# Optimization experiments

Measured on AMD Instinct MI355X. Metric: run time of the kernel, lower is better.

Reference implementation:

```python
import jax, jax.numpy as jnp
import numpy as np

B, S, H = 2, 1024, 4096
N, NOPE, ROPE, V = 64, 128, 64, 128
KV_LORA, Q_LORA = 512, 1536
QK = NOPE + ROPE  # 192
MAXPOS = 4096
SCALE = QK ** -0.5
EPS = 1e-6


def rmsnorm(x, w, eps=EPS):
    var = jnp.mean(jnp.square(x.astype(jnp.float32)), axis=-1, keepdims=True)
    return (x.astype(jnp.float32) * jax.lax.rsqrt(var + eps)).astype(x.dtype) * w


def rotate_half(x):
    x1, x2 = jnp.split(x, 2, axis=-1)
    return jnp.concatenate([-x2, x1], axis=-1)


def setup_inputs() -> dict:
    key = jax.random.key(0)
    ks = jax.random.split(key, 8)
    hidden_states = jax.random.normal(ks[0], (B, S, H), dtype=jnp.float32)
    position_ids = jnp.tile(jnp.arange(S, dtype=jnp.int64)[None, :], (B, 1))
    # real RoPE tables
    inv_freq = 1.0 / (10000.0 ** (np.arange(0, ROPE, 2, dtype=np.float32) / ROPE))
    t = np.arange(MAXPOS, dtype=np.float32)
    freqs = np.outer(t, inv_freq)
    emb = np.concatenate([freqs, freqs], axis=-1)
    cos = jnp.asarray(np.cos(emb), dtype=jnp.float32)
    sin = jnp.asarray(np.sin(emb), dtype=jnp.float32)
    def lin(k, out_f, in_f):
        return jax.random.normal(k, (out_f, in_f), dtype=jnp.float32) * (in_f ** -0.5)
    return {
        'hidden_states': hidden_states,
        'position_ids': position_ids,
        'cos': cos,
        'sin': sin,
        'q_a_w': lin(ks[1], Q_LORA, H),
        'q_a_ln_w': jnp.ones((Q_LORA,), dtype=jnp.float32),
        'q_b_w': lin(ks[2], N * QK, Q_LORA),
        'kv_a_w': lin(ks[3], KV_LORA + ROPE, H),
        'kv_a_ln_w': jnp.ones((KV_LORA,), dtype=jnp.float32),
        'kv_b_w': lin(ks[4], N * (NOPE + V), KV_LORA),
        'o_w': lin(ks[5], H, N * V),
    }


def reference(hidden_states, position_ids, cos, sin, q_a_w, q_a_ln_w, q_b_w,
              kv_a_w, kv_a_ln_w, kv_b_w, o_w):
    b, s, _ = hidden_states.shape
    # Q path: low-rank down-proj -> RMSNorm -> up-proj
    q = rmsnorm(hidden_states @ q_a_w.T, q_a_ln_w) @ q_b_w.T
    q = q.reshape(b, s, N, QK)
    q_nope, q_pe = q[..., :NOPE], q[..., NOPE:]          # [b,s,n,128],[b,s,n,64]
    # KV path: joint down-proj -> split latent / rope part
    kv_a = hidden_states @ kv_a_w.T                       # [b,s,512+64]
    compressed_kv = rmsnorm(kv_a[..., :KV_LORA], kv_a_ln_w)  # [b,s,512]
    k_pe = kv_a[..., KV_LORA:].reshape(b, s, 1, ROPE)
    # RoPE with explicit cos/sin gathered by position_ids (unsqueeze head dim=2)
    cos_p = cos[position_ids][:, :, None, :]              # [b,s,1,64]
    sin_p = sin[position_ids][:, :, None, :]
    q_pe = q_pe * cos_p + rotate_half(q_pe) * sin_p
    k_pe = k_pe * cos_p + rotate_half(k_pe) * sin_p
    k_pe = k_pe[:, :, 0, :]                               # [b,s,64]
    # Absorbed kv_b weights: W_UK [n,128,512], W_UV [n,128,512]
    W = kv_b_w.reshape(N, NOPE + V, KV_LORA)
    W_UK, W_UV = W[:, :NOPE], W[:, NOPE:]
    # Absorb W_UK into q: attention operates in latent space
    q_lat = jnp.einsum('bsnd,ndc->bsnc', q_nope, W_UK)    # [b,s,n,512]
    scores = jnp.einsum('bsnc,btc->bnst', q_lat, compressed_kv)
    scores = scores + jnp.einsum('bsnd,btd->bnst', q_pe, k_pe)
    scores = scores * SCALE
    causal = jnp.tril(jnp.ones((s, s), dtype=bool))
    scores = jnp.where(causal[None, None], scores, jnp.finfo(scores.dtype).min)
    attn = jax.nn.softmax(scores, axis=-1)                # [b,n,s,t]
    out_lat = jnp.einsum('bnst,btc->bsnc', attn, compressed_kv)
    out = jnp.einsum('bsnc,nvc->bsnv', out_lat, W_UV)     # [b,s,n,128]
    out = out.reshape(b, s, N * V) @ o_w.T
    return out
```

## Files before the change

### kernel.cpp

```cpp
#include <hip/hip_runtime.h>
#include <hip/hip_bf16.h>
#include <math.h>


#define SCALE_QK 0.07216878364870322f

typedef short bf16x8 __attribute__((ext_vector_type(8)));
typedef float f32x4  __attribute__((ext_vector_type(4)));

__global__ __launch_bounds__(256) void cast_f32_bf16(
    const float* __restrict__ src, __hip_bfloat16* __restrict__ dst, long n)
{
    long i = ((long)blockIdx.x * 256 + threadIdx.x) * 8;
    if (i >= n) return;
    float4 a = *(const float4*)(src + i);
    float4 b = *(const float4*)(src + i + 4);
    union { bf16x8 v; __hip_bfloat16 h[8]; } u;
    u.h[0] = __float2bfloat16(a.x); u.h[1] = __float2bfloat16(a.y);
    u.h[2] = __float2bfloat16(a.z); u.h[3] = __float2bfloat16(a.w);
    u.h[4] = __float2bfloat16(b.x); u.h[5] = __float2bfloat16(b.y);
    u.h[6] = __float2bfloat16(b.z); u.h[7] = __float2bfloat16(b.w);
    *(bf16x8*)(dst + i) = u.v;
}

__global__ __launch_bounds__(256) void cast_pad_kvaw(
    const float* __restrict__ src, __hip_bfloat16* __restrict__ dst)
{
    long i = ((long)blockIdx.x * 256 + threadIdx.x) * 8;
    if (i >= 640L * 4096) return;
    const int row = (int)(i >> 12);
    union { bf16x8 v; __hip_bfloat16 h[8]; } u;
    if (row < 576) {
        float4 a = *(const float4*)(src + i);
        float4 b = *(const float4*)(src + i + 4);
        u.h[0] = __float2bfloat16(a.x); u.h[1] = __float2bfloat16(a.y);
        u.h[2] = __float2bfloat16(a.z); u.h[3] = __float2bfloat16(a.w);
        u.h[4] = __float2bfloat16(b.x); u.h[5] = __float2bfloat16(b.y);
        u.h[6] = __float2bfloat16(b.z); u.h[7] = __float2bfloat16(b.w);
    } else {
        for (int j = 0; j < 8; ++j) u.h[j] = __float2bfloat16(0.f);
    }
    *(bf16x8*)(dst + i) = u.v;
}

template<int OUT_BF16>
__global__ __launch_bounds__(256) void gemm_bf16(
    const __hip_bfloat16* __restrict__ A, const __hip_bfloat16* __restrict__ B,
    void* __restrict__ Cv, int M, int N, int K)
{
    __shared__ __hip_bfloat16 Asm[128 * 32];
    __shared__ __hip_bfloat16 Bsm[128 * 32];
    const int t  = threadIdx.x;
    const int w  = t >> 6, l = t & 63;
    const int wr = w >> 1, wc = w & 1;
    const int lr = l & 15, g = l >> 4;
    const int m0 = blockIdx.y * 128, n0 = blockIdx.x * 128;
    const int srow = l >> 2;
    const int schk = l & 3;

    f32x4 acc[4][4] = {};

    for (int k0 = 0; k0 < K; k0 += 32) {
#pragma unroll
        for (int i = 0; i < 2; ++i) {
            const int ia = w * 2 + i;
            const __hip_bfloat16* ga = A + (size_t)(m0 + ia * 16 + srow) * K + k0 + schk * 8;
            __builtin_amdgcn_global_load_lds(
                (const __attribute__((address_space(1))) void*)ga,
                (__attribute__((address_space(3))) void*)(Asm + ia * 512), 16, 0, 0);
            const __hip_bfloat16* gb = B + (size_t)(n0 + ia * 16 + srow) * K + k0 + schk * 8;
            __builtin_amdgcn_global_load_lds(
                (const __attribute__((address_space(1))) void*)gb,
                (__attribute__((address_space(3))) void*)(Bsm + ia * 512), 16, 0, 0);
        }
        __syncthreads();
        bf16x8 af[4], bfr[4];
#pragma unroll
        for (int fi = 0; fi < 4; ++fi)
            af[fi] = *(const bf16x8*)(Asm + (wr * 64 + fi * 16 + lr) * 32 + g * 8);
#pragma unroll
        for (int fj = 0; fj < 4; ++fj)
            bfr[fj] = *(const bf16x8*)(Bsm + (wc * 64 + fj * 16 + lr) * 32 + g * 8);
#pragma unroll
        for (int fi = 0; fi < 4; ++fi)
#pragma unroll
            for (int fj = 0; fj < 4; ++fj)
                acc[fi][fj] = __builtin_amdgcn_mfma_f32_16x16x32_bf16(
                    af[fi], bfr[fj], acc[fi][fj], 0, 0, 0);
        __syncthreads();
    }

#pragma unroll
    for (int fi = 0; fi < 4; ++fi)
#pragma unroll
        for (int fj = 0; fj < 4; ++fj) {
            const int col = n0 + wc * 64 + fj * 16 + lr;
#pragma unroll
            for (int r = 0; r < 4; ++r) {
                const size_t row = (size_t)(m0 + wr * 64 + fi * 16 + g * 4 + r);
                if (OUT_BF16)
                    ((__hip_bfloat16*)Cv)[row * N + col] = __float2bfloat16(acc[fi][fj][r]);
                else
                    ((float*)Cv)[row * N + col] = acc[fi][fj][r];
            }
        }
}

__global__ __launch_bounds__(256) void rmsnorm_qa(
    const float* __restrict__ x, const float* __restrict__ w,
    __hip_bfloat16* __restrict__ o)
{
    __shared__ float red[4];
    const int row = blockIdx.x;
    const float* xr = x + (size_t)row * 1536;
    float ss = 0.f;
#pragma unroll
    for (int i = threadIdx.x; i < 1536; i += 256) { float v = xr[i]; ss = fmaf(v, v, ss); }
#pragma unroll
    for (int off = 1; off < 64; off <<= 1) ss += __shfl_xor(ss, off, 64);
    const int lane = threadIdx.x & 63, wid = threadIdx.x >> 6;
    if (lane == 0) red[wid] = ss;
    __syncthreads();
    ss = red[0] + red[1] + red[2] + red[3];
    const float r = rsqrtf(ss / 1536.f + 1e-6f);
#pragma unroll
    for (int i = threadIdx.x; i < 1536; i += 256)
        o[(size_t)row * 1536 + i] = __float2bfloat16(xr[i] * r * w[i]);
}

__global__ __launch_bounds__(256) void kv_norm_rope(
    const float* __restrict__ kva, const float* __restrict__ w,
    const int* __restrict__ pos, const float* __restrict__ cosT,
    const float* __restrict__ sinT, __hip_bfloat16* __restrict__ ckv,
    __hip_bfloat16* __restrict__ kpe)
{
    __shared__ float red[4];
    const int row = blockIdx.x;
    const float* xr = kva + (size_t)row * 640;
    float ss = 0.f;
#pragma unroll
    for (int i = threadIdx.x; i < 512; i += 256) { float v = xr[i]; ss = fmaf(v, v, ss); }
#pragma unroll
    for (int off = 1; off < 64; off <<= 1) ss += __shfl_xor(ss, off, 64);
    const int lane = threadIdx.x & 63, wid = threadIdx.x >> 6;
    if (lane == 0) red[wid] = ss;
    __syncthreads();
    ss = red[0] + red[1] + red[2] + red[3];
    const float r = rsqrtf(ss / 512.f + 1e-6f);
#pragma unroll
    for (int i = threadIdx.x; i < 512; i += 256)
        ckv[(size_t)row * 512 + i] = __float2bfloat16(xr[i] * r * w[i]);
    if (threadIdx.x < 64) {
        const int d = threadIdx.x;
        const int p = pos[row];
        const float xd = xr[512 + d];
        const float xp = xr[512 + (d ^ 32)];
        const float rot = (d < 32) ? -xp : xp;
        kpe[(size_t)row * 64 + d] = __float2bfloat16(xd * cosT[p * 64 + d] + rot * sinT[p * 64 + d]);
    }
}

__global__ __launch_bounds__(256) void qpe_rope_bf(
    __hip_bfloat16* __restrict__ q, const int* __restrict__ pos,
    const float* __restrict__ cosT, const float* __restrict__ sinT)
{
    const int idx = blockIdx.x * 256 + threadIdx.x;
    const int d = idx & 63;
    const int n = (idx >> 6) & 63;
    const int row = idx >> 12;
    const int p = pos[row];
    __hip_bfloat16* qp = q + (size_t)row * 12288 + n * 192 + 128;
    const float xd = __bfloat162float(qp[d]);
    const float xp = __bfloat162float(qp[d ^ 32]);
    const float rot = (d < 32) ? -xp : xp;
    qp[d] = __float2bfloat16(xd * cosT[p * 64 + d] + rot * sinT[p * 64 + d]);
}

__global__ __launch_bounds__(256) void attn_mfma(
    const __hip_bfloat16* __restrict__ q,
    const __hip_bfloat16* __restrict__ kvup,
    const __hip_bfloat16* __restrict__ kpe,
    __hip_bfloat16* __restrict__ attno)
{
    __shared__ __hip_bfloat16 Ksm[64 * 200];
    __shared__ unsigned char  Vsm[128 * 144];
    __shared__ __hip_bfloat16 Psm[4 * 16 * 72];

    const int t  = threadIdx.x;
    const int w  = t >> 6, l = t & 63;
    const int lr = l & 15, g = l >> 4;
    const int qb = blockIdx.x, n = blockIdx.y, b = blockIdx.z;
    const int qs = qb * 64;
    const size_t rowQ = (size_t)b * 1024 + qs + w * 16 + lr;

    bf16x8 qf[6];
#pragma unroll
    for (int ks = 0; ks < 6; ++ks)
        qf[ks] = *(const bf16x8*)(q + rowQ * 12288 + n * 192 + ks * 32 + g * 8);

    f32x4 oacc[8] = {};
    float m_[4], l_[4];
#pragma unroll
    for (int r = 0; r < 4; ++r) { m_[r] = -INFINITY; l_[r] = 0.f; }

    __hip_bfloat16* Pw = Psm + w * 16 * 72;

    for (int kt = 0; kt <= qb; ++kt) {
        const int ct = kt * 64;
        {
            const int tr  = t & 63;
            const int chb = (t >> 6) * 6;
            const size_t grow = (size_t)b * 1024 + ct + tr;
#pragma unroll
            for (int i = 0; i < 6; ++i) {
                const int ch = chb + i;
                bf16x8 v;
                if (ch < 16) v = *(const bf16x8*)(kvup + grow * 16384 + n * 256 + ch * 8);
                else         v = *(const bf16x8*)(kpe + grow * 64 + (ch - 16) * 8);
                *(bf16x8*)(Ksm + tr * 200 + ch * 8) = v;
            }
        }
        {
#pragma unroll
            for (int i = 0; i < 4; ++i) {
                const int cc  = t + 256 * i;
                const int tr  = cc >> 4;
                const int v0  = (cc & 15) * 8;
                const int key = cc & 7;
                const size_t grow = (size_t)b * 1024 + ct + tr;
                union { bf16x8 v; __hip_bfloat16 h[8]; } u;
                u.v = *(const bf16x8*)(kvup + grow * 16384 + n * 256 + 128 + v0);
                const int tb = (2 * tr) ^ (key << 4);
#pragma unroll
                for (int j = 0; j < 8; ++j)
                    *(__hip_bfloat16*)(Vsm + (size_t)(v0 + j) * 144 + tb) = u.h[j];
            }
        }
        __syncthreads();

        f32x4 sacc[4] = {};
#pragma unroll
        for (int ks = 0; ks < 6; ++ks)
#pragma unroll
            for (int ft = 0; ft < 4; ++ft) {
                bf16x8 kf = *(const bf16x8*)(Ksm + (ft * 16 + lr) * 200 + ks * 32 + g * 8);
                sacc[ft] = __builtin_amdgcn_mfma_f32_16x16x32_bf16(qf[ks], kf, sacc[ft], 0, 0, 0);
            }

        const bool diag = (kt == qb);
#pragma unroll
        for (int r = 0; r < 4; ++r) {
            const int qg = qs + w * 16 + g * 4 + r;
            float pv[4];
            float rmax = -3e38f;
#pragma unroll
            for (int ft = 0; ft < 4; ++ft) {
                float v = sacc[ft][r] * SCALE_QK;
                if (diag && (ct + ft * 16 + lr) > qg) v = -3e38f;
                pv[ft] = v;
                rmax = fmaxf(rmax, v);
            }
            rmax = fmaxf(rmax, __shfl_xor(rmax, 1, 64));
            rmax = fmaxf(rmax, __shfl_xor(rmax, 2, 64));
            rmax = fmaxf(rmax, __shfl_xor(rmax, 4, 64));
            rmax = fmaxf(rmax, __shfl_xor(rmax, 8, 64));
            const float mnew  = fmaxf(m_[r], rmax);
            const float alpha = __expf(m_[r] - mnew);
            m_[r] = mnew;
            float ps = 0.f;
#pragma unroll
            for (int ft = 0; ft < 4; ++ft) {
                const float e = __expf(pv[ft] - mnew);
                pv[ft] = e;
                ps += e;
            }
            ps += __shfl_xor(ps, 1, 64);
            ps += __shfl_xor(ps, 2, 64);
            ps += __shfl_xor(ps, 4, 64);
            ps += __shfl_xor(ps, 8, 64);
            l_[r] = l_[r] * alpha + ps;
#pragma unroll
            for (int fj = 0; fj < 8; ++fj) oacc[fj][r] *= alpha;
#pragma unroll
            for (int ft = 0; ft < 4; ++ft)
                Pw[(g * 4 + r) * 72 + ft * 16 + lr] = __float2bfloat16(pv[ft]);
        }

#pragma unroll
        for (int s = 0; s < 2; ++s) {
            bf16x8 pa = *(const bf16x8*)(Pw + lr * 72 + s * 32 + g * 8);
#pragma unroll
            for (int fj = 0; fj < 8; ++fj) {
                const int v = fj * 16 + lr;
                const int chunk = (((4 * s + g) ^ ((v >> 3) & 7)) << 4);
                bf16x8 bv = *(const bf16x8*)(Vsm + (size_t)v * 144 + chunk);
                oacc[fj] = __builtin_amdgcn_mfma_f32_16x16x32_bf16(pa, bv, oacc[fj], 0, 0, 0);
            }
        }
        __syncthreads();
    }

#pragma unroll
    for (int r = 0; r < 4; ++r) {
        const float inv = 1.f / l_[r];
        const size_t orow = (size_t)b * 1024 + qs + w * 16 + g * 4 + r;
#pragma unroll
        for (int fj = 0; fj < 8; ++fj)
            attno[orow * 8192 + n * 128 + fj * 16 + lr] = __float2bfloat16(oacc[fj][r] * inv);
    }
}

extern "C" void kernel_launch(void* const* d_in, const int* in_sizes, int n_in,
                              void* d_out, int out_size, void* d_ws, size_t ws_size,
                              hipStream_t stream)
{
    const float* hidden    = (const float*)d_in[0];
    const int*   pos       = (const int*)d_in[1];
    const float* cosT      = (const float*)d_in[2];
    const float* sinT      = (const float*)d_in[3];
    const float* q_a_w     = (const float*)d_in[4];
    const float* q_a_ln_w  = (const float*)d_in[5];
    const float* q_b_w     = (const float*)d_in[6];
    const float* kv_a_w    = (const float*)d_in[7];
    const float* kv_a_ln_w = (const float*)d_in[8];
    const float* kv_b_w    = (const float*)d_in[9];
    const float* o_w       = (const float*)d_in[10];
    float* out = (float*)d_out;

    char* p = (char*)d_ws;
    __hip_bfloat16* hbf      = (__hip_bfloat16*)p; p += 2048L * 4096 * 2;
    __hip_bfloat16* wbf      = (__hip_bfloat16*)p; p += 67108864;
    float*          qa_f32   = (float*)p;          p += 2048L * 1536 * 4;
    __hip_bfloat16* qa_bf    = (__hip_bfloat16*)p; p += 2048L * 1536 * 2;
    __hip_bfloat16* qbuf_bf  = (__hip_bfloat16*)p; p += 2048L * 12288 * 2;
    float*          kva_f32  = (float*)p;          p += 2048L * 640 * 4;
    __hip_bfloat16* ckv_bf   = (__hip_bfloat16*)p; p += 2048L * 512 * 2;
    __hip_bfloat16* kpe_bf   = (__hip_bfloat16*)p; p += 2048L * 64 * 2;
    __hip_bfloat16* kvup_bf  = (__hip_bfloat16*)p; p += 2048L * 16384 * 2;
    __hip_bfloat16* attno_bf = (__hip_bfloat16*)p; p += 2048L * 8192 * 2;

    auto nb8 = [](long n) { return (int)((n / 8 + 255) / 256); };

    cast_f32_bf16<<<nb8(2048L * 4096), 256, 0, stream>>>(hidden, hbf, 2048L * 4096);

    cast_f32_bf16<<<nb8(1536L * 4096), 256, 0, stream>>>(q_a_w, wbf, 1536L * 4096);
    gemm_bf16<0><<<dim3(12, 16), 256, 0, stream>>>(hbf, wbf, qa_f32, 2048, 1536, 4096);
    rmsnorm_qa<<<2048, 256, 0, stream>>>(qa_f32, q_a_ln_w, qa_bf);

    cast_f32_bf16<<<nb8(12288L * 1536), 256, 0, stream>>>(q_b_w, wbf, 12288L * 1536);
    gemm_bf16<1><<<dim3(96, 16), 256, 0, stream>>>(qa_bf, wbf, qbuf_bf, 2048, 12288, 1536);

    cast_pad_kvaw<<<nb8(640L * 4096), 256, 0, stream>>>(kv_a_w, wbf);
    gemm_bf16<0><<<dim3(5, 16), 256, 0, stream>>>(hbf, wbf, kva_f32, 2048, 640, 4096);
    kv_norm_rope<<<2048, 256, 0, stream>>>(kva_f32, kv_a_ln_w, pos, cosT, sinT, ckv_bf, kpe_bf);

    qpe_rope_bf<<<32768, 256, 0, stream>>>(qbuf_bf, pos, cosT, sinT);

    cast_f32_bf16<<<nb8(16384L * 512), 256, 0, stream>>>(kv_b_w, wbf, 16384L * 512);
    gemm_bf16<1><<<dim3(128, 16), 256, 0, stream>>>(ckv_bf, wbf, kvup_bf, 2048, 16384, 512);

    attn_mfma<<<dim3(16, 64, 2), 256, 0, stream>>>(qbuf_bf, kvup_bf, kpe_bf, attno_bf);

    cast_f32_bf16<<<nb8(4096L * 8192), 256, 0, stream>>>(o_w, wbf, 4096L * 8192);
    gemm_bf16<0><<<dim3(32, 16), 256, 0, stream>>>(attno_bf, wbf, out, 2048, 4096, 8192);
}
```

Before: 1.140 ms.

## Split-K the skinny GEMMs, add lazy softmax rescale and MFMA priority hints

Adds split-K to the q_a, kv_a and output projections: partial products go to a workspace and are summed by new reduction kernels, so the small-N GEMMs launch more blocks. The attention kernel now skips the online-softmax rescale unless the row max grows by more than 8, raises wave priority around its MFMA sections, and gets an occupancy hint in its launch bounds. The GEMM also interleaves B-fragment loads with MFMAs and gets its own occupancy hint. The cost is extra fp32 partial traffic and extra reduction launches.

```diff
diff --git a/kernel.cpp b/kernel.cpp
--- a/kernel.cpp
+++ b/kernel.cpp
@@ -43,10 +43,39 @@
     *(bf16x8*)(dst + i) = u.v;
 }
 
+__global__ __launch_bounds__(256) void reduce_sum(
+    const float* __restrict__ parts, float* __restrict__ out, long n, int S)
+{
+    long i = ((long)blockIdx.x * 256 + threadIdx.x) * 4;
+    const long stride = (long)gridDim.x * 1024;
+    for (; i < n; i += stride) {
+        float4 acc = *(const float4*)(parts + i);
+        for (int s = 1; s < S; ++s) {
+            float4 v = *(const float4*)(parts + (size_t)s * n + i);
+            acc.x += v.x; acc.y += v.y; acc.z += v.z; acc.w += v.w;
+        }
+        *(float4*)(out + i) = acc;
+    }
+}
+
+__global__ __launch_bounds__(256) void add_inplace(
+    float* __restrict__ out, const float* __restrict__ a, long n)
+{
+    long i = ((long)blockIdx.x * 256 + threadIdx.x) * 4;
+    const long stride = (long)gridDim.x * 1024;
+    for (; i < n; i += stride) {
+        float4 o = *(const float4*)(out + i);
+        float4 v = *(const float4*)(a + i);
+        o.x += v.x; o.y += v.y; o.z += v.z; o.w += v.w;
+        *(float4*)(out + i) = o;
+    }
+}
+
 template<int OUT_BF16>
-__global__ __launch_bounds__(256) void gemm_bf16(
+__global__ __launch_bounds__(256, 4) void gemm_bf16(
     const __hip_bfloat16* __restrict__ A, const __hip_bfloat16* __restrict__ B,
-    void* __restrict__ Cv, int M, int N, int K)
+    void* __restrict__ C0, float* __restrict__ Calt,
+    int M, int N, int K, int lda, int ldb)
 {
     __shared__ __hip_bfloat16 Asm[128 * 32];
     __shared__ __hip_bfloat16 Bsm[128 * 32];
@@ -55,55 +84,71 @@
     const int wr = w >> 1, wc = w & 1;
     const int lr = l & 15, g = l >> 4;
     const int m0 = blockIdx.y * 128, n0 = blockIdx.x * 128;
+    const int z  = blockIdx.z;
     const int srow = l >> 2;
     const int schk = l & 3;
 
+    const __hip_bfloat16* Az = A + (size_t)z * K;
+    const __hip_bfloat16* Bz = B + (size_t)z * K;
+
     f32x4 acc[4][4] = {};
 
     for (int k0 = 0; k0 < K; k0 += 32) {
 #pragma unroll
         for (int i = 0; i < 2; ++i) {
             const int ia = w * 2 + i;
-            const __hip_bfloat16* ga = A + (size_t)(m0 + ia * 16 + srow) * K + k0 + schk * 8;
+            const __hip_bfloat16* ga = Az + (size_t)(m0 + ia * 16 + srow) * lda + k0 + schk * 8;
             __builtin_amdgcn_global_load_lds(
                 (const __attribute__((address_space(1))) void*)ga,
                 (__attribute__((address_space(3))) void*)(Asm + ia * 512), 16, 0, 0);
-            const __hip_bfloat16* gb = B + (size_t)(n0 + ia * 16 + srow) * K + k0 + schk * 8;
+            const __hip_bfloat16* gb = Bz + (size_t)(n0 + ia * 16 + srow) * ldb + k0 + schk * 8;
             __builtin_amdgcn_global_load_lds(
                 (const __attribute__((address_space(1))) void*)gb,
                 (__attribute__((address_space(3))) void*)(Bsm + ia * 512), 16, 0, 0);
         }
         __syncthreads();
-        bf16x8 af[4], bfr[4];
+        bf16x8 af[4];
 #pragma unroll
         for (int fi = 0; fi < 4; ++fi)
             af[fi] = *(const bf16x8*)(Asm + (wr * 64 + fi * 16 + lr) * 32 + g * 8);
 #pragma unroll
-        for (int fj = 0; fj < 4; ++fj)
-            bfr[fj] = *(const bf16x8*)(Bsm + (wc * 64 + fj * 16 + lr) * 32 + g * 8);
+        for (int fj = 0; fj < 4; ++fj) {
+            bf16x8 bfr = *(const bf16x8*)(Bsm + (wc * 64 + fj * 16 + lr) * 32 + g * 8);
+#pragma unroll
+            for (int fi = 0; fi < 4; ++fi)
+                acc[fi][fj] = __builtin_amdgcn_mfma_f32_16x16x32_bf16(
+                    af[fi], bfr, acc[fi][fj], 0, 0, 0);
+        }
+        __syncthreads();
+    }
+
+    if (OUT_BF16) {
+        __hip_bfloat16* C = (__hip_bfloat16*)C0;
 #pragma unroll
         for (int fi = 0; fi < 4; ++fi)
 #pragma unroll
-            for (int fj = 0; fj < 4; ++fj)
-                acc[fi][fj] = __builtin_amdgcn_mfma_f32_16x16x32_bf16(
-                    af[fi], bfr[fj], acc[fi][fj], 0, 0, 0);
-        __syncthreads();
-    }
-
-#pragma unroll
-    for (int fi = 0; fi < 4; ++fi)
-#pragma unroll
-        for (int fj = 0; fj < 4; ++fj) {
-            const int col = n0 + wc * 64 + fj * 16 + lr;
-#pragma unroll
-            for (int r = 0; r < 4; ++r) {
-                const size_t row = (size_t)(m0 + wr * 64 + fi * 16 + g * 4 + r);
-                if (OUT_BF16)
-                    ((__hip_bfloat16*)Cv)[row * N + col] = __float2bfloat16(acc[fi][fj][r]);
-                else
-                    ((float*)Cv)[row * N + col] = acc[fi][fj][r];
-            }
-        }
+            for (int fj = 0; fj < 4; ++fj) {
+                const int col = n0 + wc * 64 + fj * 16 + lr;
+#pragma unroll
+                for (int r = 0; r < 4; ++r) {
+                    const size_t row = (size_t)(m0 + wr * 64 + fi * 16 + g * 4 + r);
+                    C[row * N + col] = __float2bfloat16(acc[fi][fj][r]);
+                }
+            }
+    } else {
+        float* C = (z == 0) ? (float*)C0 : (Calt + (size_t)(z - 1) * M * N);
+#pragma unroll
+        for (int fi = 0; fi < 4; ++fi)
+#pragma unroll
+            for (int fj = 0; fj < 4; ++fj) {
+                const int col = n0 + wc * 64 + fj * 16 + lr;
+#pragma unroll
+                for (int r = 0; r < 4; ++r) {
+                    const size_t row = (size_t)(m0 + wr * 64 + fi * 16 + g * 4 + r);
+                    C[row * N + col] = acc[fi][fj][r];
+                }
+            }
+    }
 }
 
 __global__ __launch_bounds__(256) void rmsnorm_qa(
@@ -176,7 +221,7 @@
     qp[d] = __float2bfloat16(xd * cosT[p * 64 + d] + rot * sinT[p * 64 + d]);
 }
 
-__global__ __launch_bounds__(256) void attn_mfma(
+__global__ __launch_bounds__(256, 3) void attn_mfma(
     const __hip_bfloat16* __restrict__ q,
     const __hip_bfloat16* __restrict__ kvup,
     const __hip_bfloat16* __restrict__ kpe,
@@ -239,6 +284,7 @@
         __syncthreads();
 
         f32x4 sacc[4] = {};
+        __builtin_amdgcn_s_setprio(1);
 #pragma unroll
         for (int ks = 0; ks < 6; ++ks)
 #pragma unroll
@@ -246,6 +292,7 @@
                 bf16x8 kf = *(const bf16x8*)(Ksm + (ft * 16 + lr) * 200 + ks * 32 + g * 8);
                 sacc[ft] = __builtin_amdgcn_mfma_f32_16x16x32_bf16(qf[ks], kf, sacc[ft], 0, 0, 0);
             }
+        __builtin_amdgcn_s_setprio(0);
 
         const bool diag = (kt == qb);
 #pragma unroll
@@ -264,13 +311,18 @@
             rmax = fmaxf(rmax, __shfl_xor(rmax, 2, 64));
             rmax = fmaxf(rmax, __shfl_xor(rmax, 4, 64));
             rmax = fmaxf(rmax, __shfl_xor(rmax, 8, 64));
-            const float mnew  = fmaxf(m_[r], rmax);
-            const float alpha = __expf(m_[r] - mnew);
-            m_[r] = mnew;
+            if (!__all(rmax - m_[r] <= 8.f)) {
+                const float mnew  = fmaxf(m_[r], rmax);
+                const float alpha = __expf(m_[r] - mnew);
+                m_[r] = mnew;
+                l_[r] *= alpha;
+#pragma unroll
+                for (int fj = 0; fj < 8; ++fj) oacc[fj][r] *= alpha;
+            }
             float ps = 0.f;
 #pragma unroll
             for (int ft = 0; ft < 4; ++ft) {
-                const float e = __expf(pv[ft] - mnew);
+                const float e = __expf(pv[ft] - m_[r]);
                 pv[ft] = e;
                 ps += e;
             }
@@ -278,14 +330,13 @@
             ps += __shfl_xor(ps, 2, 64);
             ps += __shfl_xor(ps, 4, 64);
             ps += __shfl_xor(ps, 8, 64);
-            l_[r] = l_[r] * alpha + ps;
-#pragma unroll
-            for (int fj = 0; fj < 8; ++fj) oacc[fj][r] *= alpha;
+            l_[r] += ps;
 #pragma unroll
             for (int ft = 0; ft < 4; ++ft)
                 Pw[(g * 4 + r) * 72 + ft * 16 + lr] = __float2bfloat16(pv[ft]);
         }
 
+        __builtin_amdgcn_s_setprio(1);
 #pragma unroll
         for (int s = 0; s < 2; ++s) {
             bf16x8 pa = *(const bf16x8*)(Pw + lr * 72 + s * 32 + g * 8);
@@ -297,6 +348,7 @@
                 oacc[fj] = __builtin_amdgcn_mfma_f32_16x16x32_bf16(pa, bv, oacc[fj], 0, 0, 0);
             }
         }
+        __builtin_amdgcn_s_setprio(0);
         __syncthreads();
     }
 
@@ -330,6 +382,7 @@
     char* p = (char*)d_ws;
     __hip_bfloat16* hbf      = (__hip_bfloat16*)p; p += 2048L * 4096 * 2;
     __hip_bfloat16* wbf      = (__hip_bfloat16*)p; p += 67108864;
+    float*          parts    = (float*)p;          p += 2048L * 1536 * 4 * 4;
     float*          qa_f32   = (float*)p;          p += 2048L * 1536 * 4;
     __hip_bfloat16* qa_bf    = (__hip_bfloat16*)p; p += 2048L * 1536 * 2;
     __hip_bfloat16* qbuf_bf  = (__hip_bfloat16*)p; p += 2048L * 12288 * 2;
@@ -344,23 +397,30 @@
     cast_f32_bf16<<<nb8(2048L * 4096), 256, 0, stream>>>(hidden, hbf, 2048L * 4096);
 
     cast_f32_bf16<<<nb8(1536L * 4096), 256, 0, stream>>>(q_a_w, wbf, 1536L * 4096);
-    gemm_bf16<0><<<dim3(12, 16), 256, 0, stream>>>(hbf, wbf, qa_f32, 2048, 1536, 4096);
+    gemm_bf16<0><<<dim3(12, 16, 4), 256, 0, stream>>>(hbf, wbf, parts, parts + 2048L * 1536,
+                                                      2048, 1536, 1024, 4096, 4096);
+    reduce_sum<<<2048, 256, 0, stream>>>(parts, qa_f32, 2048L * 1536, 4);
     rmsnorm_qa<<<2048, 256, 0, stream>>>(qa_f32, q_a_ln_w, qa_bf);
 
+    cast_pad_kvaw<<<nb8(640L * 4096), 256, 0, stream>>>(kv_a_w, wbf);
+    gemm_bf16<0><<<dim3(5, 16, 8), 256, 0, stream>>>(hbf, wbf, parts, parts + 2048L * 640,
+                                                     2048, 640, 512, 4096, 4096);
+    reduce_sum<<<1280, 256, 0, stream>>>(parts, kva_f32, 2048L * 640, 8);
+    kv_norm_rope<<<2048, 256, 0, stream>>>(kva_f32, kv_a_ln_w, pos, cosT, sinT, ckv_bf, kpe_bf);
+
     cast_f32_bf16<<<nb8(12288L * 1536), 256, 0, stream>>>(q_b_w, wbf, 12288L * 1536);
-    gemm_bf16<1><<<dim3(96, 16), 256, 0, stream>>>(qa_bf, wbf, qbuf_bf, 2048, 12288, 1536);
-
-    cast_pad_kvaw<<<nb8(640L * 4096), 256, 0, stream>>>(kv_a_w, wbf);
-    gemm_bf16<0><<<dim3(5, 16), 256, 0, stream>>>(hbf, wbf, kva_f32, 2048, 640, 4096);
-    kv_norm_rope<<<2048, 256, 0, stream>>>(kva_f32, kv_a_ln_w, pos, cosT, sinT, ckv_bf, kpe_bf);
-
+    gemm_bf16<1><<<dim3(96, 16, 1), 256, 0, stream>>>(qa_bf, wbf, qbuf_bf, nullptr,
+                                                      2048, 12288, 1536, 1536, 1536);
     qpe_rope_bf<<<32768, 256, 0, stream>>>(qbuf_bf, pos, cosT, sinT);
 
     cast_f32_bf16<<<nb8(16384L * 512), 256, 0, stream>>>(kv_b_w, wbf, 16384L * 512);
-    gemm_bf16<1><<<dim3(128, 16), 256, 0, stream>>>(ckv_bf, wbf, kvup_bf, 2048, 16384, 512);
+    gemm_bf16<1><<<dim3(128, 16, 1), 256, 0, stream>>>(ckv_bf, wbf, kvup_bf, nullptr,
+                                                       2048, 16384, 512, 512, 512);
 
     attn_mfma<<<dim3(16, 64, 2), 256, 0, stream>>>(qbuf_bf, kvup_bf, kpe_bf, attno_bf);
 
     cast_f32_bf16<<<nb8(4096L * 8192), 256, 0, stream>>>(o_w, wbf, 4096L * 8192);
-    gemm_bf16<0><<<dim3(32, 16), 256, 0, stream>>>(attno_bf, wbf, out, 2048, 4096, 8192);
-}
+    gemm_bf16<0><<<dim3(32, 16, 2), 256, 0, stream>>>(attno_bf, wbf, out, parts,
+                                                      2048, 4096, 4096, 8192, 8192);
+    add_inplace<<<2048, 256, 0, stream>>>(out, parts, 2048L * 4096);
+}
```

Result: slower. 1.311 ms (+15.0%).
